# Performance work log

Hardware: AMD Instinct MI355X
Metric: run time of the kernel (lower is better)

Reference implementation:

```python
import jax, jax.numpy as jnp
import numpy as np

B, L = 256, 8192
DIM, NPAT, HIST, WIN = 256, 64, 32, 8


def setup_inputs() -> dict:
    key = jax.random.key(0)
    ks = jax.random.split(key, 6)
    return {
        "x": jax.random.normal(ks[0], (B, L), dtype=jnp.float32),
        "avg_init": jax.random.normal(ks[1], (B, NPAT), dtype=jnp.float32),
        "conv_w": jax.random.normal(ks[2], (DIM, 1, HIST), dtype=jnp.float32) * 0.1,
        "conv_b": jax.random.normal(ks[3], (DIM,), dtype=jnp.float32) * 0.1,
        "keys_w": jax.random.normal(ks[4], (NPAT, DIM), dtype=jnp.float32) * 0.1,
        "shapes_w": jax.random.normal(ks[5], (WIN, NPAT), dtype=jnp.float32) * 0.1,
    }


def reference(x, avg_init, conv_w, conv_b, keys_w, shapes_w):
    b, l = x.shape
    n_pat = keys_w.shape[0]
    hist = conv_w.shape[2]
    win = shapes_w.shape[0]

    # randn avg_scores, centered (module draws fresh randn each forward; we take it as input)
    avg0 = avg_init - jnp.mean(avg_init, axis=-1, keepdims=True)

    padded = jnp.pad(x, ((0, 0), (hist - 1, 0)))[:, None, :]  # [B,1,L+hist-1]
    out = jax.lax.conv_general_dilated(
        padded, conv_w, window_strides=(win,), padding="VALID",
        dimension_numbers=("NCH", "OIH", "NCH"))
    out = out + conv_b[None, :, None]                     # [B,dim,T]
    out = jnp.transpose(out, (2, 0, 1))                   # [T,B,dim]

    # relu6(keys(out)) -> attn scores [T,B,n_pat]
    scores = jnp.clip(jnp.einsum("tbd,pd->tbp", out, keys_w), 0.0, 6.0)

    # sequential balanced-routing scan over T with running average scores
    def step(avg, score):                                 # avg,score: [B,n_pat]
        idx = jnp.argmax(score - avg, axis=-1)
        prob = jax.nn.one_hot(idx, n_pat, dtype=score.dtype)
        return avg + prob - 1.0 / n_pat, prob

    _, probs = jax.lax.scan(step, avg0, scores)           # probs: [T,B,n_pat]
    probs = jnp.transpose(probs, (1, 0, 2))               # [B,T,n_pat]

    signal = jnp.einsum("btp,wp->btw", probs, shapes_w).reshape(b, -1)[:, :l]
    return jax.nn.relu(signal - x)
```

## Files before the change

### kernel.cpp

```cpp
#include <hip/hip_runtime.h>


constexpr int Bb = 256, Ll = 8192, DIMc = 256, NPAT = 64, HIST = 32, WINc = 8;
constexpr int Tt = Ll / WINc;
constexpr int TC = 32;
constexpr int NC = Tt / TC;
constexpr float CINV = 1.0f / 64.0f;

#define DPP_STAGE(m, ctrl, rmask)                                              \
  (m) = fmaxf((m), __int_as_float(__builtin_amdgcn_update_dpp(                 \
            __float_as_int(m), __float_as_int(m), (ctrl), (rmask), 0xF, false)))

#define DPP_ADDF(s, ctrl, rmask)                                               \
  do {                                                                         \
    int _si = __float_as_int(s);                                               \
    int _ti = __builtin_amdgcn_update_dpp(_si, _si, (ctrl), (rmask), 0xF, false); \
    (s) += __int_as_float(_ti);                                                \
  } while (0)

#if defined(__has_builtin)
#if __has_builtin(__builtin_amdgcn_permlane16_swap)
#define HAVE_PL16 1
#endif
#if __has_builtin(__builtin_amdgcn_permlane32_swap)
#define HAVE_PL32 1
#endif
#if __has_builtin(__builtin_amdgcn_fmed3f)
#define HAVE_MED3 1
#endif
#endif

__device__ __forceinline__ float clamp01(float t) {
#if defined(HAVE_MED3)
  return __builtin_amdgcn_fmed3f(t, 0.0f, 1.0f);
#else
  return fminf(fmaxf(t, 0.0f), 1.0f);
#endif
}

__device__ __forceinline__ float wave_max64(float v, int lane) {
  float m = v;
  DPP_STAGE(m, 0xB1, 0xF);
  DPP_STAGE(m, 0x4E, 0xF);
  DPP_STAGE(m, 0x141, 0xF);
  DPP_STAGE(m, 0x140, 0xF);
#if defined(HAVE_PL16)
  {
    auto r = __builtin_amdgcn_permlane16_swap(__float_as_int(m),
                                              __float_as_int(m), false, false);
    m = fmaxf(__int_as_float(r[0]), __int_as_float(r[1]));
  }
#else
  m = fmaxf(m, __int_as_float(
                   __builtin_amdgcn_ds_swizzle(__float_as_int(m), 0x401F)));
#endif
#if defined(HAVE_PL32)
  {
    auto r = __builtin_amdgcn_permlane32_swap(__float_as_int(m),
                                              __float_as_int(m), false, false);
    m = fmaxf(__int_as_float(r[0]), __int_as_float(r[1]));
  }
#else
  m = fmaxf(m, __int_as_float(__builtin_amdgcn_ds_bpermute(
                   ((lane ^ 32) << 2), __float_as_int(m))));
#endif
  return m;
}

__global__ __launch_bounds__(256) void precompute_kernel(
    const float* __restrict__ conv_w, const float* __restrict__ conv_b,
    const float* __restrict__ keys_w, float* __restrict__ wsf) {
  __shared__ float part[8][32];
  __shared__ float bred[4];
  const int p = blockIdx.x;
  const int t = threadIdx.x;
  const int h = t & 31, g = t >> 5;
  const float* kwp = keys_w + (size_t)p * DIMc;

  float acc = 0.f;
#pragma unroll
  for (int dd = 0; dd < 32; ++dd) {
    int d = g * 32 + dd;
    acc = fmaf(kwp[d], conv_w[d * HIST + h], acc);
  }
  part[g][h] = acc;

  float bp = kwp[t] * conv_b[t];
#pragma unroll
  for (int off = 32; off; off >>= 1) bp += __shfl_down(bp, off);
  if ((t & 63) == 0) bred[t >> 6] = bp;
  __syncthreads();

  if (t < 32) {
    float s = 0.f;
#pragma unroll
    for (int gg = 0; gg < 8; ++gg) s += part[gg][t];
    wsf[(t >> 2) * (NPAT * 4) + p * 4 + (t & 3)] = s;
  } else if (t == 32) {
    wsf[NPAT * HIST + p] = (bred[0] + bred[1]) + (bred[2] + bred[3]);
  }
}

__global__ __launch_bounds__(256) void shaper_kernel(
    const float* __restrict__ x, const float* __restrict__ avg_init,
    const float* __restrict__ shapes_w, const float* __restrict__ wsf,
    float* __restrict__ out) {
  __shared__ __align__(16) float xpad[HIST - 1 + Ll + 1];
  __shared__ float scb[2][TC * NPAT];
  __shared__ unsigned int bmbuf[2][64];
  __shared__ unsigned char idx8[Tt];
  __shared__ float shp[WINc * NPAT];

  const int b    = blockIdx.x;
  const int tid  = threadIdx.x;
  const int wid  = tid >> 6;
  const int lane = tid & 63;
  const float* xrow = x + (size_t)b * Ll;

  if (tid < HIST - 1) xpad[tid] = 0.f;
  {
    const float4* xv4 = (const float4*)xrow;
#pragma unroll
    for (int k = 0; k < 8; ++k) {
      int i4 = k * 256 + tid;
      float4 v = xv4[i4];
      float* dst = xpad + HIST - 1 + i4 * 4;
      dst[0] = v.x; dst[1] = v.y; dst[2] = v.z; dst[3] = v.w;
    }
  }
  for (int i = tid; i < WINc * NPAT; i += 256) shp[i] = shapes_w[i];

  float av0;
  {
    float s = avg_init[(size_t)b * NPAT + lane];
    float t = s;
    DPP_ADDF(t, 0xB1, 0xF);
    DPP_ADDF(t, 0x4E, 0xF);
    DPP_ADDF(t, 0x141, 0xF);
    DPP_ADDF(t, 0x140, 0xF);
    DPP_ADDF(t, 0x142, 0xA);
    DPP_ADDF(t, 0x143, 0xC);
    float tot = __int_as_float(__builtin_amdgcn_readlane(__float_as_int(t), 63));
    av0 = s - tot * CINV;
  }

  __syncthreads();

  constexpr float SC75 = 37778931862957161709568.0f;

  if (wid == 0) {
    float C = 0.f;
    __syncthreads();

    for (int c = 0; c < NC; ++c) {
      const float* sb = scb[c & 1];
      float U[TC];
#pragma unroll
      for (int i = 0; i < TC; ++i) U[i] = sb[i * NPAT + lane];
      float bmlo = 0.f, bmhi = 0.f;
      float v  = U[0] - C;
      float pA = U[1] - C;
#pragma unroll
      for (int i = 0; i < TC; ++i) {
        float g  = wave_max64(v, lane);
        float d  = g - v;
        float t2 = __builtin_fmaf(d * SC75, -SC75, 1.0f);
        float e  = clamp01(t2);
        C += e;
        if (i < 16) bmlo = __builtin_fmaf(e, (float)(1u << i), bmlo);
        else        bmhi = __builtin_fmaf(e, (float)(1u << (i - 16)), bmhi);
        if (i + 1 < TC) {
          v = pA - e;
          if (i + 2 < TC) pA = U[i + 2] - C;
        }
      }
      bmbuf[c & 1][lane] = (unsigned int)bmlo | ((unsigned int)bmhi << 16);
      __syncthreads();
    }
    __syncthreads();
  } else {
    float4 w2v[8];
    {
      const float4* w2g = (const float4*)wsf;
#pragma unroll
      for (int h4 = 0; h4 < 8; ++h4) w2v[h4] = w2g[h4 * 64 + lane];
    }
    float b2 = wsf[NPAT * HIST + lane];

    auto fill = [&](int c, float* __restrict__ sb) {
      int base = c * TC;
      for (int tl = wid - 1; tl < TC; tl += 3) {
        int t = base + tl;
        const float4* xw = (const float4*)(xpad + t * WINc);
        float acc = b2;
#pragma unroll
        for (int h4 = 0; h4 < 8; ++h4) {
          float4 xv = xw[h4];
          float4 wv = w2v[h4];
          acc = fmaf(xv.x, wv.x, acc);
          acc = fmaf(xv.y, wv.y, acc);
          acc = fmaf(xv.z, wv.z, acc);
          acc = fmaf(xv.w, wv.w, acc);
        }
        float sc = fminf(fmaxf(acc, 0.f), 6.f);
        sb[tl * NPAT + lane] = (sc - av0) + (float)t * CINV;
      }
    };

    auto extract3 = [&](int cc) {
      unsigned int mv = bmbuf[cc & 1][lane];
      for (int i = wid - 1; i < TC; i += 3) {
        unsigned long long mk = __ballot(((mv >> i) & 1u) != 0u);
        int w = (int)(__ffsll(mk) - 1);
        if (lane == 0) idx8[cc * TC + i] = (unsigned char)w;
      }
    };

    fill(0, scb[0]);
    __syncthreads();

    for (int c = 0; c < NC; ++c) {
      if (c + 1 < NC) fill(c + 1, scb[(c + 1) & 1]);
      if (c >= 1) extract3(c - 1);
      __syncthreads();
    }
    extract3(NC - 1);
    __syncthreads();
  }

  float4* outv = (float4*)(out + (size_t)b * Ll);
#pragma unroll
  for (int k = 0; k < 8; ++k) {
    int i4 = k * 256 + tid;
    int l0 = i4 * 4;
    int t  = l0 >> 3;
    int w0 = l0 & 7;
    int p  = (int)idx8[t];
    float4 o;
    o.x = fmaxf(shp[(w0 + 0) * NPAT + p] - xpad[HIST - 1 + l0 + 0], 0.f);
    o.y = fmaxf(shp[(w0 + 1) * NPAT + p] - xpad[HIST - 1 + l0 + 1], 0.f);
    o.z = fmaxf(shp[(w0 + 2) * NPAT + p] - xpad[HIST - 1 + l0 + 2], 0.f);
    o.w = fmaxf(shp[(w0 + 3) * NPAT + p] - xpad[HIST - 1 + l0 + 3], 0.f);
    outv[i4] = o;
  }
}

extern "C" void kernel_launch(void* const* d_in, const int* in_sizes, int n_in,
                              void* d_out, int out_size, void* d_ws, size_t ws_size,
                              hipStream_t stream) {
  const float* x        = (const float*)d_in[0];
  const float* avg_init = (const float*)d_in[1];
  const float* conv_w   = (const float*)d_in[2];
  const float* conv_b   = (const float*)d_in[3];
  const float* keys_w   = (const float*)d_in[4];
  const float* shapes_w = (const float*)d_in[5];
  float* wsf = (float*)d_ws;

  precompute_kernel<<<NPAT, 256, 0, stream>>>(conv_w, conv_b, keys_w, wsf);
  shaper_kernel<<<Bb, 256, 0, stream>>>(x, avg_init, shapes_w, wsf,
                                        (float*)d_out);
}
```

Before: 170.9 us.

## Pipeline routing scan with top-2 wave reductions to break serial dependency

Replaces the per-step wave max reduction in the sequential routing scan with a top-2 reduction computed one step ahead, so the reduction for step i+1 can start before step i's winner is known. The winner is then resolved by ballots: if the previous winner also holds the current max, the second-best is chosen when it beats max minus one. This is meant to shorten the loop-carried critical path of the single-wave scan. In exchange each reduction carries two values, and the code adds ballots and inline-asm selects; exact ties and the equality-based winner detection could differ from argmax semantics.

```diff
diff --git a/kernel.cpp b/kernel.cpp
--- a/kernel.cpp
+++ b/kernel.cpp
@@ -6,10 +6,6 @@
 constexpr int TC = 32;
 constexpr int NC = Tt / TC;
 constexpr float CINV = 1.0f / 64.0f;
-
-#define DPP_STAGE(m, ctrl, rmask)                                              \
-  (m) = fmaxf((m), __int_as_float(__builtin_amdgcn_update_dpp(                 \
-            __float_as_int(m), __float_as_int(m), (ctrl), (rmask), 0xF, false)))
 
 #define DPP_ADDF(s, ctrl, rmask)                                               \
   do {                                                                         \
@@ -25,46 +21,88 @@
 #if __has_builtin(__builtin_amdgcn_permlane32_swap)
 #define HAVE_PL32 1
 #endif
-#if __has_builtin(__builtin_amdgcn_fmed3f)
-#define HAVE_MED3 1
-#endif
-#endif
-
-__device__ __forceinline__ float clamp01(float t) {
-#if defined(HAVE_MED3)
-  return __builtin_amdgcn_fmed3f(t, 0.0f, 1.0f);
-#else
-  return fminf(fmaxf(t, 0.0f), 1.0f);
-#endif
-}
-
-__device__ __forceinline__ float wave_max64(float v, int lane) {
-  float m = v;
-  DPP_STAGE(m, 0xB1, 0xF);
-  DPP_STAGE(m, 0x4E, 0xF);
-  DPP_STAGE(m, 0x141, 0xF);
-  DPP_STAGE(m, 0x140, 0xF);
+#endif
+
+__device__ __forceinline__ float sel_f(float a, float b, unsigned long long m) {
+  float r;
+  asm("v_cndmask_b32 %0, %1, %2, %3" : "=v"(r) : "v"(a), "v"(b), "s"(m));
+  return r;
+}
+__device__ __forceinline__ unsigned sel_u(unsigned a, unsigned b,
+                                          unsigned long long m) {
+  unsigned r;
+  asm("v_cndmask_b32 %0, %1, %2, %3" : "=v"(r) : "v"(a), "v"(b), "s"(m));
+  return r;
+}
+
+__device__ __forceinline__ void top2_64(float h, float& A, float& B) {
+  float m = h;
+  float s = __int_as_float(0xff800000);
+#define T2_DPP(ctrl)                                                           \
+  {                                                                            \
+    int mi = __float_as_int(m), si = __float_as_int(s);                        \
+    float tm = __int_as_float(                                                 \
+        __builtin_amdgcn_update_dpp(mi, mi, (ctrl), 0xF, 0xF, false));         \
+    float ts = __int_as_float(                                                 \
+        __builtin_amdgcn_update_dpp(si, si, (ctrl), 0xF, 0xF, false));         \
+    float mn = fminf(m, tm);                                                   \
+    m = fmaxf(m, tm);                                                          \
+    s = fmaxf(fmaxf(s, ts), mn);                                               \
+  }
+  T2_DPP(0xB1)
+  T2_DPP(0x4E)
+  T2_DPP(0x141)
+  T2_DPP(0x140)
+#undef T2_DPP
 #if defined(HAVE_PL16)
   {
     auto r = __builtin_amdgcn_permlane16_swap(__float_as_int(m),
                                               __float_as_int(m), false, false);
-    m = fmaxf(__int_as_float(r[0]), __int_as_float(r[1]));
+    auto rs = __builtin_amdgcn_permlane16_swap(__float_as_int(s),
+                                               __float_as_int(s), false, false);
+    float a = __int_as_float(r[0]), b = __int_as_float(r[1]);
+    float sa = __int_as_float(rs[0]), sb = __int_as_float(rs[1]);
+    float mn = fminf(a, b);
+    m = fmaxf(a, b);
+    s = fmaxf(fmaxf(sa, sb), mn);
   }
 #else
-  m = fmaxf(m, __int_as_float(
-                   __builtin_amdgcn_ds_swizzle(__float_as_int(m), 0x401F)));
+  {
+    float tm = __int_as_float(
+        __builtin_amdgcn_ds_swizzle(__float_as_int(m), 0x401F));
+    float ts = __int_as_float(
+        __builtin_amdgcn_ds_swizzle(__float_as_int(s), 0x401F));
+    float mn = fminf(m, tm);
+    m = fmaxf(m, tm);
+    s = fmaxf(fmaxf(s, ts), mn);
+  }
 #endif
 #if defined(HAVE_PL32)
   {
     auto r = __builtin_amdgcn_permlane32_swap(__float_as_int(m),
                                               __float_as_int(m), false, false);
-    m = fmaxf(__int_as_float(r[0]), __int_as_float(r[1]));
+    auto rs = __builtin_amdgcn_permlane32_swap(__float_as_int(s),
+                                               __float_as_int(s), false, false);
+    float a = __int_as_float(r[0]), b = __int_as_float(r[1]);
+    float sa = __int_as_float(rs[0]), sb = __int_as_float(rs[1]);
+    float mn = fminf(a, b);
+    m = fmaxf(a, b);
+    s = fmaxf(fmaxf(sa, sb), mn);
   }
 #else
-  m = fmaxf(m, __int_as_float(__builtin_amdgcn_ds_bpermute(
-                   ((lane ^ 32) << 2), __float_as_int(m))));
-#endif
-  return m;
+  {
+    int lane = (int)(threadIdx.x & 63);
+    float tm = __int_as_float(__builtin_amdgcn_ds_bpermute(
+        ((lane ^ 32) << 2), __float_as_int(m)));
+    float ts = __int_as_float(__builtin_amdgcn_ds_bpermute(
+        ((lane ^ 32) << 2), __float_as_int(s)));
+    float mn = fminf(m, tm);
+    m = fmaxf(m, tm);
+    s = fmaxf(fmaxf(s, ts), mn);
+  }
+#endif
+  A = m;
+  B = s;
 }
 
 __global__ __launch_bounds__(256) void precompute_kernel(
@@ -146,35 +184,55 @@
 
   __syncthreads();
 
-  constexpr float SC75 = 37778931862957161709568.0f;
-
   if (wid == 0) {
     float C = 0.f;
     __syncthreads();
 
     for (int c = 0; c < NC; ++c) {
       const float* sb = scb[c & 1];
-      float U[TC];
-#pragma unroll
-      for (int i = 0; i < TC; ++i) U[i] = sb[i * NPAT + lane];
-      float bmlo = 0.f, bmhi = 0.f;
-      float v  = U[0] - C;
-      float pA = U[1] - C;
-#pragma unroll
-      for (int i = 0; i < TC; ++i) {
-        float g  = wave_max64(v, lane);
-        float d  = g - v;
-        float t2 = __builtin_fmaf(d * SC75, -SC75, 1.0f);
-        float e  = clamp01(t2);
-        C += e;
-        if (i < 16) bmlo = __builtin_fmaf(e, (float)(1u << i), bmlo);
-        else        bmhi = __builtin_fmaf(e, (float)(1u << (i - 16)), bmhi);
-        if (i + 1 < TC) {
-          v = pA - e;
-          if (i + 2 < TC) pA = U[i + 2] - C;
+      float ur[8];
+#pragma unroll
+      for (int k = 0; k < 8; ++k) ur[k] = sb[k * NPAT + lane];
+      unsigned bm = 0u;
+      unsigned long long mprev = 0ull;
+
+      float h0 = ur[0] - C;
+      float h1 = ur[1] - C;
+      float A0, B0, A1, B1;
+      top2_64(h0, A0, B0);
+      top2_64(h1, A1, B1);
+      {
+        unsigned long long mwin = __ballot(h0 == A0);
+        float C1 = C + 1.0f;
+        C = sel_f(C, C1, mwin);
+        bm = sel_u(bm, bm | 1u, mwin);
+        mprev = mwin;
+        h0 = ur[2] - C;
+        top2_64(h0, A0, B0);
+      }
+
+#pragma unroll
+      for (int i = 1; i < TC; ++i) {
+        if (i + 7 < TC) ur[(i + 7) & 7] = sb[(i + 7) * NPAT + lane];
+        float hC = (i & 1) ? h1 : h0;
+        float Ac = (i & 1) ? A1 : A0;
+        float Bc = (i & 1) ? B1 : B0;
+        unsigned long long mH  = __ballot(hC == Ac);
+        unsigned long long mH2 = __ballot(hC == Bc);
+        bool gt = __ballot(Bc > Ac - 1.0f) != 0ull;
+        unsigned long long mwin =
+            ((mH & mprev) != 0ull) ? (gt ? mH2 : mH) : mH;
+        float C1 = C + 1.0f;
+        C = sel_f(C, C1, mwin);
+        bm = sel_u(bm, bm | (1u << i), mwin);
+        mprev = mwin;
+        if (i + 2 < TC) {
+          float hn = ur[(i + 2) & 7] - C;
+          if (i & 1) { h1 = hn; top2_64(h1, A1, B1); }
+          else       { h0 = hn; top2_64(h0, A0, B0); }
         }
       }
-      bmbuf[c & 1][lane] = (unsigned int)bmlo | ((unsigned int)bmhi << 16);
+      bmbuf[c & 1][lane] = bm;
       __syncthreads();
     }
     __syncthreads();
```

After: 212.6 us. 24.4% more time.

## Process two scan steps per wave reduction using top-two max tracking

Applied to the files above, without the earlier changes.

The serial routing scan now packs two patterns per lane and two consecutive time steps into one wave, computing a joint top-1/top-2 reduction. The second step's argmax is derived from the first step's max and runner-up, adjusted when the winner's running average changes. This halves the number of full cross-lane reductions on the critical sequential path. In exchange, each reduction carries two values, there are more selects and a ballot per step pair, and tie handling becomes subtler.

```diff
diff --git a/kernel.cpp b/kernel.cpp
--- a/kernel.cpp
+++ b/kernel.cpp
@@ -6,10 +6,6 @@
 constexpr int TC = 32;
 constexpr int NC = Tt / TC;
 constexpr float CINV = 1.0f / 64.0f;
-
-#define DPP_STAGE(m, ctrl, rmask)                                              \
-  (m) = fmaxf((m), __int_as_float(__builtin_amdgcn_update_dpp(                 \
-            __float_as_int(m), __float_as_int(m), (ctrl), (rmask), 0xF, false)))
 
 #define DPP_ADDF(s, ctrl, rmask)                                               \
   do {                                                                         \
@@ -22,9 +18,6 @@
 #if __has_builtin(__builtin_amdgcn_permlane16_swap)
 #define HAVE_PL16 1
 #endif
-#if __has_builtin(__builtin_amdgcn_permlane32_swap)
-#define HAVE_PL32 1
-#endif
 #if __has_builtin(__builtin_amdgcn_fmed3f)
 #define HAVE_MED3 1
 #endif
@@ -38,33 +31,9 @@
 #endif
 }
 
-__device__ __forceinline__ float wave_max64(float v, int lane) {
-  float m = v;
-  DPP_STAGE(m, 0xB1, 0xF);
-  DPP_STAGE(m, 0x4E, 0xF);
-  DPP_STAGE(m, 0x141, 0xF);
-  DPP_STAGE(m, 0x140, 0xF);
-#if defined(HAVE_PL16)
-  {
-    auto r = __builtin_amdgcn_permlane16_swap(__float_as_int(m),
-                                              __float_as_int(m), false, false);
-    m = fmaxf(__int_as_float(r[0]), __int_as_float(r[1]));
-  }
-#else
-  m = fmaxf(m, __int_as_float(
-                   __builtin_amdgcn_ds_swizzle(__float_as_int(m), 0x401F)));
-#endif
-#if defined(HAVE_PL32)
-  {
-    auto r = __builtin_amdgcn_permlane32_swap(__float_as_int(m),
-                                              __float_as_int(m), false, false);
-    m = fmaxf(__int_as_float(r[0]), __int_as_float(r[1]));
-  }
-#else
-  m = fmaxf(m, __int_as_float(__builtin_amdgcn_ds_bpermute(
-                   ((lane ^ 32) << 2), __float_as_int(m))));
-#endif
-  return m;
+__device__ __forceinline__ float emask(float d) {
+  constexpr float SC75 = 37778931862957161709568.0f;
+  return clamp01(__builtin_fmaf(d * SC75, -SC75, 1.0f));
 }
 
 __global__ __launch_bounds__(256) void precompute_kernel(
@@ -146,35 +115,115 @@
 
   __syncthreads();
 
-  constexpr float SC75 = 37778931862957161709568.0f;
-
   if (wid == 0) {
-    float C = 0.f;
+    const int  l5 = lane & 31;
+    const bool hi = (lane >= 32);
+    float C0 = 0.f, C1 = 0.f;
     __syncthreads();
 
     for (int c = 0; c < NC; ++c) {
       const float* sb = scb[c & 1];
-      float U[TC];
-#pragma unroll
-      for (int i = 0; i < TC; ++i) U[i] = sb[i * NPAT + lane];
-      float bmlo = 0.f, bmhi = 0.f;
-      float v  = U[0] - C;
-      float pA = U[1] - C;
-#pragma unroll
-      for (int i = 0; i < TC; ++i) {
-        float g  = wave_max64(v, lane);
-        float d  = g - v;
-        float t2 = __builtin_fmaf(d * SC75, -SC75, 1.0f);
-        float e  = clamp01(t2);
-        C += e;
-        if (i < 16) bmlo = __builtin_fmaf(e, (float)(1u << i), bmlo);
-        else        bmhi = __builtin_fmaf(e, (float)(1u << (i - 16)), bmhi);
-        if (i + 1 < TC) {
-          v = pA - e;
-          if (i + 2 < TC) pA = U[i + 2] - C;
+      float2 ur[8];
+#pragma unroll
+      for (int t = 0; t < 8; ++t)
+        ur[t] = *(const float2*)(sb + t * NPAT + 2 * l5);
+      float bm0lo = 0.f, bm0hi = 0.f, bm1lo = 0.f, bm1hi = 0.f;
+
+#pragma unroll
+      for (int k = 0; k < 16; ++k) {
+        const int t0 = 2 * k, t1 = 2 * k + 1;
+        float2 u0 = ur[t0 & 7];
+        float2 u1 = ur[t1 & 7];
+        if (t0 + 8 < TC) ur[t0 & 7] = *(const float2*)(sb + (t0 + 8) * NPAT + 2 * l5);
+        if (t1 + 8 < TC) ur[t1 & 7] = *(const float2*)(sb + (t1 + 8) * NPAT + 2 * l5);
+        float v0 = u0.x - C0, v1 = u0.y - C1;
+        float h0 = u1.x - C0, h1 = u1.y - C1;
+        float x0 = hi ? h0 : v0;
+        float x1 = hi ? h1 : v1;
+        float m = fmaxf(x0, x1);
+        float s = fminf(x0, x1);
+#define T2HOP(ctrl)                                                            \
+        {                                                                      \
+          int mi = __float_as_int(m), si = __float_as_int(s);                  \
+          float tm = __int_as_float(                                           \
+              __builtin_amdgcn_update_dpp(mi, mi, (ctrl), 0xF, 0xF, false));   \
+          float ts = __int_as_float(                                           \
+              __builtin_amdgcn_update_dpp(si, si, (ctrl), 0xF, 0xF, false));   \
+          float mn = fminf(m, tm);                                             \
+          m = fmaxf(m, tm);                                                    \
+          s = fmaxf(fmaxf(s, ts), mn);                                         \
+        }
+        T2HOP(0xB1)
+        T2HOP(0x4E)
+        T2HOP(0x141)
+        T2HOP(0x140)
+#undef T2HOP
+#if defined(HAVE_PL16)
+        {
+          auto r  = __builtin_amdgcn_permlane16_swap(__float_as_int(m),
+                                                     __float_as_int(m), false, false);
+          auto rs = __builtin_amdgcn_permlane16_swap(__float_as_int(s),
+                                                     __float_as_int(s), false, false);
+          float a = __int_as_float(r[0]),  b2 = __int_as_float(r[1]);
+          float sa = __int_as_float(rs[0]), sb2 = __int_as_float(rs[1]);
+          float mn = fminf(a, b2);
+          m = fmaxf(a, b2);
+          s = fmaxf(fmaxf(sa, sb2), mn);
+        }
+#else
+        {
+          float tm = __int_as_float(
+              __builtin_amdgcn_ds_swizzle(__float_as_int(m), 0x401F));
+          float ts = __int_as_float(
+              __builtin_amdgcn_ds_swizzle(__float_as_int(s), 0x401F));
+          float mn = fminf(m, tm);
+          m = fmaxf(m, tm);
+          s = fmaxf(fmaxf(s, ts), mn);
+        }
+#endif
+        float pM = __int_as_float(__builtin_amdgcn_ds_bpermute(
+            ((lane ^ 32) << 2), __float_as_int(m)));
+        float pS = __int_as_float(__builtin_amdgcn_ds_bpermute(
+            ((lane ^ 32) << 2), __float_as_int(s)));
+        float A_v = hi ? pM : m;
+        float A_h = hi ? m : pM;
+        float B_h = hi ? s : pS;
+
+        float e0 = emask(A_v - v0);
+        float e1 = emask(A_v - v1);
+        C0 += e0; C1 += e1;
+        if (k < 8) {
+          bm0lo = __builtin_fmaf(e0, (float)(1u << t0), bm0lo);
+          bm1lo = __builtin_fmaf(e1, (float)(1u << t0), bm1lo);
+        } else {
+          bm0hi = __builtin_fmaf(e0, (float)(1u << (t0 - 16)), bm0hi);
+          bm1hi = __builtin_fmaf(e1, (float)(1u << (t0 - 16)), bm1hi);
+        }
+        float mh0 = emask(A_h - h0);
+        float mh1 = emask(A_h - h1);
+        float q = __builtin_fmaf(e1, mh1, e0 * mh0);
+        unsigned long long mq = __ballot(q > 0.0f);
+        float galt = fmaxf(A_h - 1.0f, B_h);
+        float gmax = (mq != 0ull) ? galt : A_h;
+        float w0 = h0 - e0;
+        float w1 = h1 - e1;
+        float f0 = emask(gmax - w0);
+        float f1 = emask(gmax - w1);
+        C0 += f0; C1 += f1;
+        if (k < 8) {
+          bm0lo = __builtin_fmaf(f0, (float)(1u << t1), bm0lo);
+          bm1lo = __builtin_fmaf(f1, (float)(1u << t1), bm1lo);
+        } else {
+          bm0hi = __builtin_fmaf(f0, (float)(1u << (t1 - 16)), bm0hi);
+          bm1hi = __builtin_fmaf(f1, (float)(1u << (t1 - 16)), bm1hi);
         }
       }
-      bmbuf[c & 1][lane] = (unsigned int)bmlo | ((unsigned int)bmhi << 16);
+      if (lane < 32) {
+        bmbuf[c & 1][2 * l5 + 0] =
+            (unsigned int)bm0lo | ((unsigned int)bm0hi << 16);
+        bmbuf[c & 1][2 * l5 + 1] =
+            (unsigned int)bm1lo | ((unsigned int)bm1hi << 16);
+      }
       __syncthreads();
     }
     __syncthreads();
```

New measurement: 181.0 us. 1.06x slower.
